# Optimization experiments

Hardware: AMD Instinct MI355X
Metric: run time of the kernel (lower is better)

## Reference

```python
import jax, jax.numpy as jnp
from jax import lax
import numpy as np

B, C, H, W = 32, 256, 64, 64
K = 5            # ECA kernel size for C=256
HID = 64         # fusion hidden = C//4
E_LAMBDA = 1e-4


def setup_inputs() -> dict:
    key = jax.random.key(0)
    k1, k2, k3, k4 = jax.random.split(key, 4)
    x = jax.random.normal(k1, (B, C, H, W), dtype=jnp.float32)
    conv_w = jax.random.normal(k2, (1, 1, K), dtype=jnp.float32) * 0.3
    w1 = jax.random.normal(k3, (HID, C), dtype=jnp.float32) * (1.0 / np.sqrt(C))
    w2 = jax.random.normal(k4, (C, HID), dtype=jnp.float32) * (1.0 / np.sqrt(HID))
    return {"x": x, "conv_w": conv_w, "w1": w1, "w2": w2}


def reference(x, conv_w, w1, w2):
    b, c, h, w = x.shape
    # --- shared per-channel mean (used by both ECA's GAP and SimAM) ---
    mean_c = x.mean(axis=(2, 3))                       # [B, C]

    # --- ECA branch: 1D conv over channel dim of GAP, sigmoid gate ---
    y = lax.conv_general_dilated(
        mean_c[:, None, :], conv_w,
        window_strides=(1,), padding=[((K - 1) // 2, (K - 1) // 2)],
        dimension_numbers=("NCH", "OIH", "NCH"))      # [B, 1, C]
    eca_gate = jax.nn.sigmoid(y)[:, 0, :, None, None]  # [B, C, 1, 1]
    x_eca = x * eca_gate

    # --- SimAM branch ---
    n = h * w - 1
    d = x - mean_c[:, :, None, None]                   # [B, C, H, W]
    var = jnp.sum(d * d, axis=(2, 3), keepdims=True) / n
    energy = d * d / (4.0 * (var + E_LAMBDA)) + 0.5
    x_simam = x * jax.nn.sigmoid(energy)

    # --- fusion gate: GAP of (eca+simam) -> 2-layer MLP -> sigmoid ---
    gap = (x_eca + x_simam).mean(axis=(2, 3))          # [B, C]
    hid = jax.nn.relu(gap @ w1.T)                      # [B, HID]
    alpha = jax.nn.sigmoid(hid @ w2.T)[:, :, None, None]  # [B, C, 1, 1]

    return alpha * x_simam + (1.0 - alpha) * x_eca
```

## Files before the change

kernel.cpp:

```cpp
#include <hip/hip_runtime.h>
#include <math.h>

#define Bdim 32
#define Cdim 256
#define Hdim 64
#define Wdim 64
#define HW   (Hdim * Wdim)
#define KS   5
#define HID  64
#define E_LAMBDA 1e-4f

typedef float vfloat4 __attribute__((ext_vector_type(4)));

__device__ __forceinline__ float sigmoidf(float v) {
    return __builtin_amdgcn_rcpf(1.0f + __expf(-v));
}

__global__ __launch_bounds__(256) void stats_gate_kernel(
        const float* __restrict__ x,
        const float* __restrict__ conv_w,
        const float* __restrict__ w1,
        const float* __restrict__ w2,
        float* __restrict__ mean_out,
        float* __restrict__ inv_out,
        float* __restrict__ ssum_out,
        float* __restrict__ gate_out,
        float* __restrict__ alpha_out,
        int*   __restrict__ counter) {
    const int bc = blockIdx.x;
    const int b  = bc >> 8;
    const vfloat4* __restrict__ x4 = (const vfloat4*)(x + (size_t)bc * HW);
    const int t = threadIdx.x;
    const int lane = t & 63;
    const int wid  = t >> 6;

    __shared__ float red[8];
    __shared__ float bcast[2];
    __shared__ int   slast;

    vfloat4 v[4];
    float sum = 0.0f, sq = 0.0f;
#pragma unroll
    for (int i = 0; i < 4; ++i) {
        v[i] = x4[t + 256 * i];
        sum += v[i].x + v[i].y + v[i].z + v[i].w;
        sq  += v[i].x * v[i].x + v[i].y * v[i].y
             + v[i].z * v[i].z + v[i].w * v[i].w;
    }
#pragma unroll
    for (int off = 32; off > 0; off >>= 1) {
        sum += __shfl_down(sum, off);
        sq  += __shfl_down(sq, off);
    }
    if (lane == 0) { red[wid] = sum; red[4 + wid] = sq; }
    __syncthreads();
    if (t == 0) {
        const float ts = red[0] + red[1] + red[2] + red[3];
        const float tq = red[4] + red[5] + red[6] + red[7];
        const float mn  = ts * (1.0f / HW);
        const float var = (tq - ts * ts * (1.0f / HW)) * (1.0f / (HW - 1));
        const float iv  = 0.25f / (var + E_LAMBDA);
        __hip_atomic_store(&mean_out[bc], mn, __ATOMIC_RELAXED,
                           __HIP_MEMORY_SCOPE_AGENT);
        inv_out[bc] = iv;
        bcast[0] = mn;
        bcast[1] = iv;
    }
    __syncthreads();
    const float mn  = bcast[0];
    const float inv = bcast[1];

    float p = 0.0f;
#pragma unroll
    for (int i = 0; i < 4; ++i) {
        float d;
        d = v[i].x - mn; p += v[i].x * sigmoidf(d * d * inv + 0.5f);
        d = v[i].y - mn; p += v[i].y * sigmoidf(d * d * inv + 0.5f);
        d = v[i].z - mn; p += v[i].z * sigmoidf(d * d * inv + 0.5f);
        d = v[i].w - mn; p += v[i].w * sigmoidf(d * d * inv + 0.5f);
    }
#pragma unroll
    for (int off = 32; off > 0; off >>= 1) p += __shfl_down(p, off);
    if (lane == 0) red[wid] = p;
    __syncthreads();

    if (t == 0) {
        __hip_atomic_store(&ssum_out[bc], red[0] + red[1] + red[2] + red[3],
                           __ATOMIC_RELAXED, __HIP_MEMORY_SCOPE_AGENT);
        asm volatile("s_waitcnt vmcnt(0)" ::: "memory");
        const int old = __hip_atomic_fetch_add(&counter[b], 1, __ATOMIC_RELAXED,
                                               __HIP_MEMORY_SCOPE_AGENT);
        slast = (old == Cdim - 1);
    }
    __syncthreads();
    if (!slast) return;

    __shared__ float sm[Cdim];
    __shared__ float sgap[Cdim];
    __shared__ float shid[HID];

    const float mb = __hip_atomic_load(&mean_out[b * Cdim + t],
                                       __ATOMIC_RELAXED, __HIP_MEMORY_SCOPE_AGENT);
    const float sb = __hip_atomic_load(&ssum_out[b * Cdim + t],
                                       __ATOMIC_RELAXED, __HIP_MEMORY_SCOPE_AGENT);
    sm[t] = mb;
    __syncthreads();

    float acc = 0.0f;
#pragma unroll
    for (int k = 0; k < KS; ++k) {
        const int cc = t + k - (KS - 1) / 2;
        const float mv = (cc >= 0 && cc < Cdim) ? sm[cc] : 0.0f;
        acc += conv_w[k] * mv;
    }
    const float gate = sigmoidf(acc);
    gate_out[b * Cdim + t] = gate;
    sgap[t] = gate * mb + sb * (1.0f / HW);
    __syncthreads();

    if (t < HID) {
        const vfloat4* __restrict__ w14 = (const vfloat4*)(w1 + t * Cdim);
        const vfloat4* __restrict__ g4  = (const vfloat4*)sgap;
        float h = 0.0f;
#pragma unroll
        for (int i = 0; i < Cdim / 4; ++i) {
            const vfloat4 wv = w14[i];
            const vfloat4 gv = g4[i];
            h += wv.x * gv.x + wv.y * gv.y + wv.z * gv.z + wv.w * gv.w;
        }
        shid[t] = fmaxf(h, 0.0f);
    }
    __syncthreads();

    {
        const vfloat4* __restrict__ w24 = (const vfloat4*)(w2 + t * HID);
        const vfloat4* __restrict__ h4  = (const vfloat4*)shid;
        float a = 0.0f;
#pragma unroll
        for (int j = 0; j < HID / 4; ++j) {
            const vfloat4 wv = w24[j];
            const vfloat4 hv = h4[j];
            a += wv.x * hv.x + wv.y * hv.y + wv.z * hv.z + wv.w * hv.w;
        }
        alpha_out[b * Cdim + t] = sigmoidf(a);
    }
}

__global__ __launch_bounds__(256) void final_kernel(
        const float* __restrict__ x,
        const float* __restrict__ mean_c,
        const float* __restrict__ inv_c,
        const float* __restrict__ eca,
        const float* __restrict__ alpha,
        float* __restrict__ out) {
    const int bc = blockIdx.x;
    const float mn  = mean_c[bc];
    const float inv = inv_c[bc];
    const float g   = eca[bc];
    const float a   = alpha[bc];
    const float one_minus_a_g = (1.0f - a) * g;

    const vfloat4* __restrict__ x4 = (const vfloat4*)(x + (size_t)bc * HW);
    vfloat4* __restrict__ o4 = (vfloat4*)(out + (size_t)bc * HW);
    const int t = threadIdx.x;

    vfloat4 v[4];
#pragma unroll
    for (int i = 0; i < 4; ++i) v[i] = x4[t + 256 * i];

#pragma unroll
    for (int i = 0; i < 4; ++i) {
        vfloat4 r;
        float d;
        d = v[i].x - mn; r.x = v[i].x * (a * sigmoidf(d * d * inv + 0.5f) + one_minus_a_g);
        d = v[i].y - mn; r.y = v[i].y * (a * sigmoidf(d * d * inv + 0.5f) + one_minus_a_g);
        d = v[i].z - mn; r.z = v[i].z * (a * sigmoidf(d * d * inv + 0.5f) + one_minus_a_g);
        d = v[i].w - mn; r.w = v[i].w * (a * sigmoidf(d * d * inv + 0.5f) + one_minus_a_g);
        __builtin_nontemporal_store(r, &o4[t + 256 * i]);
    }
}

extern "C" void kernel_launch(void* const* d_in, const int* in_sizes, int n_in,
                              void* d_out, int out_size, void* d_ws, size_t ws_size,
                              hipStream_t stream) {
    const float* x      = (const float*)d_in[0];
    const float* conv_w = (const float*)d_in[1];
    const float* w1     = (const float*)d_in[2];
    const float* w2     = (const float*)d_in[3];
    float* out = (float*)d_out;

    const int BC = Bdim * Cdim;
    float* mean_c = (float*)d_ws;
    float* inv_c  = mean_c + BC;
    float* ssum   = inv_c + BC;
    float* eca    = ssum + BC;
    float* alpha  = eca + BC;
    int*   cnt    = (int*)(alpha + BC);

    hipMemsetAsync(cnt, 0, Bdim * sizeof(int), stream);

    stats_gate_kernel<<<BC, 256, 0, stream>>>(x, conv_w, w1, w2,
                                              mean_c, inv_c, ssum, eca, alpha, cnt);
    final_kernel<<<BC, 256, 0, stream>>>(x, mean_c, inv_c, eca, alpha, out);
}
```

Before: 311.6 us.

## Drop atomic last-block gate and recompute MLP gate per block in final kernel

Removes the atomic counter, the memset and the last-block-per-batch gate computation from the stats kernel, leaving it a pure stats pass. The final kernel now recomputes the ECA conv, the 2-layer MLP and the per-channel alpha for its batch inside every block, while its x loads are already in flight. This drops the cross-block synchronization, a memset launch and the serialized tail. The cost is redundant work in every block: the w1 matvec reads the full 64 KB w1 matrix from cache each time, and that runs through the gate path before the elementwise output stage.

```diff
diff --git a/kernel.cpp b/kernel.cpp
--- a/kernel.cpp
+++ b/kernel.cpp
@@ -16,27 +16,14 @@
     return __builtin_amdgcn_rcpf(1.0f + __expf(-v));
 }
 
-__global__ __launch_bounds__(256) void stats_gate_kernel(
+__global__ __launch_bounds__(256) void stats_kernel(
         const float* __restrict__ x,
-        const float* __restrict__ conv_w,
-        const float* __restrict__ w1,
-        const float* __restrict__ w2,
         float* __restrict__ mean_out,
         float* __restrict__ inv_out,
-        float* __restrict__ ssum_out,
-        float* __restrict__ gate_out,
-        float* __restrict__ alpha_out,
-        int*   __restrict__ counter) {
+        float* __restrict__ ssum_out) {
     const int bc = blockIdx.x;
-    const int b  = bc >> 8;
     const vfloat4* __restrict__ x4 = (const vfloat4*)(x + (size_t)bc * HW);
     const int t = threadIdx.x;
-    const int lane = t & 63;
-    const int wid  = t >> 6;
-
-    __shared__ float red[8];
-    __shared__ float bcast[2];
-    __shared__ int   slast;
 
     vfloat4 v[4];
     float sum = 0.0f, sq = 0.0f;
@@ -47,11 +34,17 @@
         sq  += v[i].x * v[i].x + v[i].y * v[i].y
              + v[i].z * v[i].z + v[i].w * v[i].w;
     }
+
 #pragma unroll
     for (int off = 32; off > 0; off >>= 1) {
         sum += __shfl_down(sum, off);
         sq  += __shfl_down(sq, off);
     }
+
+    __shared__ float red[8];
+    __shared__ float bcast[2];
+    const int lane = t & 63;
+    const int wid  = t >> 6;
     if (lane == 0) { red[wid] = sum; red[4 + wid] = sq; }
     __syncthreads();
     if (t == 0) {
@@ -60,9 +53,8 @@
         const float mn  = ts * (1.0f / HW);
         const float var = (tq - ts * ts * (1.0f / HW)) * (1.0f / (HW - 1));
         const float iv  = 0.25f / (var + E_LAMBDA);
-        __hip_atomic_store(&mean_out[bc], mn, __ATOMIC_RELAXED,
-                           __HIP_MEMORY_SCOPE_AGENT);
-        inv_out[bc] = iv;
+        mean_out[bc] = mn;
+        inv_out[bc]  = iv;
         bcast[0] = mn;
         bcast[1] = iv;
     }
@@ -83,26 +75,35 @@
     for (int off = 32; off > 0; off >>= 1) p += __shfl_down(p, off);
     if (lane == 0) red[wid] = p;
     __syncthreads();
+    if (t == 0) ssum_out[bc] = red[0] + red[1] + red[2] + red[3];
+}
 
-    if (t == 0) {
-        __hip_atomic_store(&ssum_out[bc], red[0] + red[1] + red[2] + red[3],
-                           __ATOMIC_RELAXED, __HIP_MEMORY_SCOPE_AGENT);
-        asm volatile("s_waitcnt vmcnt(0)" ::: "memory");
-        const int old = __hip_atomic_fetch_add(&counter[b], 1, __ATOMIC_RELAXED,
-                                               __HIP_MEMORY_SCOPE_AGENT);
-        slast = (old == Cdim - 1);
-    }
-    __syncthreads();
-    if (!slast) return;
+__global__ __launch_bounds__(256) void final_fused_kernel(
+        const float* __restrict__ x,
+        const float* __restrict__ mean_c,
+        const float* __restrict__ inv_c,
+        const float* __restrict__ ssum,
+        const float* __restrict__ conv_w,
+        const float* __restrict__ w1,
+        const float* __restrict__ w2,
+        float* __restrict__ out) {
+    const int bc = blockIdx.x;
+    const int b  = bc >> 8;
+    const int c  = bc & (Cdim - 1);
+    const int t  = threadIdx.x;
+
+    const vfloat4* __restrict__ x4 = (const vfloat4*)(x + (size_t)bc * HW);
+    vfloat4 v[4];
+#pragma unroll
+    for (int i = 0; i < 4; ++i) v[i] = x4[t + 256 * i];
 
     __shared__ float sm[Cdim];
     __shared__ float sgap[Cdim];
+    __shared__ float sgate[Cdim];
     __shared__ float shid[HID];
 
-    const float mb = __hip_atomic_load(&mean_out[b * Cdim + t],
-                                       __ATOMIC_RELAXED, __HIP_MEMORY_SCOPE_AGENT);
-    const float sb = __hip_atomic_load(&ssum_out[b * Cdim + t],
-                                       __ATOMIC_RELAXED, __HIP_MEMORY_SCOPE_AGENT);
+    const float mb = mean_c[b * Cdim + t];
+    const float sb = ssum[b * Cdim + t];
     sm[t] = mb;
     __syncthreads();
 
@@ -113,9 +114,9 @@
         const float mv = (cc >= 0 && cc < Cdim) ? sm[cc] : 0.0f;
         acc += conv_w[k] * mv;
     }
-    const float gate = sigmoidf(acc);
-    gate_out[b * Cdim + t] = gate;
-    sgap[t] = gate * mb + sb * (1.0f / HW);
+    const float g_t = sigmoidf(acc);
+    sgate[t] = g_t;
+    sgap[t] = g_t * mb + sb * (1.0f / HW);
     __syncthreads();
 
     if (t < HID) {
@@ -132,50 +133,31 @@
     }
     __syncthreads();
 
+    float a = 0.0f;
     {
-        const vfloat4* __restrict__ w24 = (const vfloat4*)(w2 + t * HID);
+        const vfloat4* __restrict__ w24 = (const vfloat4*)(w2 + c * HID);
         const vfloat4* __restrict__ h4  = (const vfloat4*)shid;
-        float a = 0.0f;
 #pragma unroll
         for (int j = 0; j < HID / 4; ++j) {
             const vfloat4 wv = w24[j];
             const vfloat4 hv = h4[j];
             a += wv.x * hv.x + wv.y * hv.y + wv.z * hv.z + wv.w * hv.w;
         }
-        alpha_out[b * Cdim + t] = sigmoidf(a);
     }
-}
+    const float alpha = sigmoidf(a);
+    const float mn  = sm[c];
+    const float inv = inv_c[bc];
+    const float omg = (1.0f - alpha) * sgate[c];
 
-__global__ __launch_bounds__(256) void final_kernel(
-        const float* __restrict__ x,
-        const float* __restrict__ mean_c,
-        const float* __restrict__ inv_c,
-        const float* __restrict__ eca,
-        const float* __restrict__ alpha,
-        float* __restrict__ out) {
-    const int bc = blockIdx.x;
-    const float mn  = mean_c[bc];
-    const float inv = inv_c[bc];
-    const float g   = eca[bc];
-    const float a   = alpha[bc];
-    const float one_minus_a_g = (1.0f - a) * g;
-
-    const vfloat4* __restrict__ x4 = (const vfloat4*)(x + (size_t)bc * HW);
     vfloat4* __restrict__ o4 = (vfloat4*)(out + (size_t)bc * HW);
-    const int t = threadIdx.x;
-
-    vfloat4 v[4];
-#pragma unroll
-    for (int i = 0; i < 4; ++i) v[i] = x4[t + 256 * i];
-
 #pragma unroll
     for (int i = 0; i < 4; ++i) {
         vfloat4 r;
         float d;
-        d = v[i].x - mn; r.x = v[i].x * (a * sigmoidf(d * d * inv + 0.5f) + one_minus_a_g);
-        d = v[i].y - mn; r.y = v[i].y * (a * sigmoidf(d * d * inv + 0.5f) + one_minus_a_g);
-        d = v[i].z - mn; r.z = v[i].z * (a * sigmoidf(d * d * inv + 0.5f) + one_minus_a_g);
-        d = v[i].w - mn; r.w = v[i].w * (a * sigmoidf(d * d * inv + 0.5f) + one_minus_a_g);
+        d = v[i].x - mn; r.x = v[i].x * (alpha * sigmoidf(d * d * inv + 0.5f) + omg);
+        d = v[i].y - mn; r.y = v[i].y * (alpha * sigmoidf(d * d * inv + 0.5f) + omg);
+        d = v[i].z - mn; r.z = v[i].z * (alpha * sigmoidf(d * d * inv + 0.5f) + omg);
+        d = v[i].w - mn; r.w = v[i].w * (alpha * sigmoidf(d * d * inv + 0.5f) + omg);
         __builtin_nontemporal_store(r, &o4[t + 256 * i]);
     }
 }
@@ -193,13 +175,8 @@
     float* mean_c = (float*)d_ws;
     float* inv_c  = mean_c + BC;
     float* ssum   = inv_c + BC;
-    float* eca    = ssum + BC;
-    float* alpha  = eca + BC;
-    int*   cnt    = (int*)(alpha + BC);
 
-    hipMemsetAsync(cnt, 0, Bdim * sizeof(int), stream);
-
-    stats_gate_kernel<<<BC, 256, 0, stream>>>(x, conv_w, w1, w2,
-                                              mean_c, inv_c, ssum, eca, alpha, cnt);
-    final_kernel<<<BC, 256, 0, stream>>>(x, mean_c, inv_c, eca, alpha, out);
+    stats_kernel<<<BC, 256, 0, stream>>>(x, mean_c, inv_c, ssum);
+    final_fused_kernel<<<BC, 256, 0, stream>>>(x, mean_c, inv_c, ssum,
+                                               conv_w, w1, w2, out);
 }
```

New measurement: 290.4 us. 1.07x faster.
